# Kernel tuning notes

Hardware: AMD Instinct MI355X
Metric: run time of the kernel (lower is better)

## Reference

```python
import jax, jax.numpy as jnp
import numpy as np

B, L, D, ORDER, POS, HID, LMAX = 4, 4096, 1024, 2, 65, 64, 4096
K2 = (POS - 1) // 2

def _layernorm(x, w, b, eps=1e-5):
    m = jnp.mean(x, -1, keepdims=True)
    v = jnp.mean((x - m) ** 2, -1, keepdims=True)
    return (x - m) * jax.lax.rsqrt(v + eps) * w + b

def _fftconv(x, h, d):
    # torch: rfft(h, 2L, norm='forward') * rfft(x, 2L) -> irfft(.., norm='forward')
    # net scaling equals standard (unnormalized fwd / 1-over-n inverse) circular conv,
    # which is exactly jnp.fft default conventions.
    n = 2 * x.shape[-1]
    y = jnp.fft.irfft(jnp.fft.rfft(x, n=n) * jnp.fft.rfft(h, n=n), n=n)[..., : x.shape[-1]]
    return y + x * d

def setup_inputs() -> dict:
    key = jax.random.key(0)
    ks = jax.random.split(key, 12)
    s = 0.05
    # PositionalEncoding buffers/params (deterministic init, as in torch __init__)
    t = np.linspace(0, 1, LMAX, dtype=np.float64)[:, None]
    t_pos = np.arange(LMAX, dtype=np.float64)[:, None]
    k = np.arange(K2, dtype=np.float64)[None, :]
    z = np.exp(1j * 2 * np.pi * k * t_pos / LMAX)
    pos_z = np.concatenate([t, z.real, z.imag], axis=-1).astype(np.float32)  # (LMAX, POS)
    pos_t = t.reshape(1, 1, LMAX).astype(np.float32)
    # ExponentialDecayWindow alphas (deterministic init)
    max_decay = np.log(0.01) / 0.3
    min_decay = np.log(0.01) / 1.5
    alphas = np.linspace(min_decay, max_decay, D).reshape(1, D, 1).astype(np.float32)
    H3 = (ORDER + 1) * D
    return dict(
        u=jax.random.normal(ks[0], (B, L, D), jnp.float32),
        norm1_w=jnp.ones((D,), jnp.float32), norm1_b=jnp.zeros((D,), jnp.float32),
        proj_w=jax.random.normal(ks[1], (H3, D), jnp.float32) * s,
        proj_b=jnp.zeros((H3,), jnp.float32),
        conv_w=jax.random.normal(ks[2], (H3, 1, 3), jnp.float32) * 0.3,
        conv_b=jnp.zeros((H3,), jnp.float32),
        pos_t=jnp.asarray(pos_t), pos_z=jnp.asarray(pos_z),
        fnn_w0=jax.random.normal(ks[3], (HID, POS), jnp.float32) * s,
        fnn_b0=jnp.zeros((HID,), jnp.float32),
        freq0=8.0 * jnp.ones((1, HID), jnp.float32),
        fnn_w1=jax.random.normal(ks[4], (HID, HID), jnp.float32) * s,
        fnn_b1=jnp.zeros((HID,), jnp.float32),
        freq1=8.0 * jnp.ones((1, HID), jnp.float32),
        fnn_w2=jax.random.normal(ks[5], (HID, HID), jnp.float32) * s,
        fnn_b2=jnp.zeros((HID,), jnp.float32),
        freq2=8.0 * jnp.ones((1, HID), jnp.float32),
        fnn_wout=jax.random.normal(ks[6], (ORDER * D, HID), jnp.float32) * s,
        alphas=jnp.asarray(alphas),
        hy_bias=jax.random.normal(ks[7], (ORDER, 1, D, 1), jnp.float32),
        norm2_w=jnp.ones((D,), jnp.float32), norm2_b=jnp.zeros((D,), jnp.float32),
        fc_w=jax.random.normal(ks[8], (D, D), jnp.float32) * s,
        fc_b=jnp.zeros((D,), jnp.float32),
    )

def reference(u, norm1_w, norm1_b, proj_w, proj_b, conv_w, conv_b, pos_t, pos_z,
              fnn_w0, fnn_b0, freq0, fnn_w1, fnn_b1, freq1, fnn_w2, fnn_b2, freq2,
              fnn_wout, alphas, hy_bias, norm2_w, norm2_b, fc_w, fc_b):
    Lq = u.shape[1]
    # Projection: LN -> Linear -> depthwise short conv (causal-ish, pad=2, slice :L)
    x = _layernorm(u, norm1_w, norm1_b)
    x = jnp.einsum('bld,hd->blh', x, proj_w) + proj_b          # (B,L,3D)
    x = x.transpose(0, 2, 1)                                   # (B,3D,L)
    x = jax.lax.conv_general_dilated(
        x, conv_w, window_strides=(1,), padding=[(2, 2)],
        feature_group_count=x.shape[1],
        dimension_numbers=('NCH', 'OIH', 'NCH'))[..., :Lq] + conv_b[None, :, None]
    # HyenaFilter: sin-MLP over positional features, then exp-decay window
    zf = pos_z[:Lq]                                            # (L,POS)
    h = jnp.sin(freq0 * (zf @ fnn_w0.T + fnn_b0))
    h = jnp.sin(freq1 * (h @ fnn_w1.T + fnn_b1))
    h = jnp.sin(freq2 * (h @ fnn_w2.T + fnn_b2))
    h = (h @ fnn_wout.T).T.reshape(ORDER, D, Lq)               # (order,D,L)
    decay = jnp.exp(alphas * pos_t[..., :Lq])                  # (1,D,L)
    h = h * decay
    # order-wise gated FFT long convolution (faithful to torch chunk/broadcast semantics)
    v = x[:, -1:, :]                                           # (B,1,L)
    for i in range(ORDER):
        v = x[:, i:i + 1, :] * _fftconv(v, h[i][None], hy_bias[i])  # (B,D,L)
    y = u + v.transpose(0, 2, 1)
    out = _layernorm(y, norm2_w, norm2_b) @ fc_w.T + fc_b      # activation = identity
    return out + y
```

## Files before the change

kernel.cpp:

```cpp
#include <hip/hip_runtime.h>
#include <hip/hip_bf16.h>

#define LL 4096
#define DD 1024
#define NB 4
#define N4 4096
#define KBINS 4097
#define NSLOT4 4366
#define PI_F 3.14159265358979323846f
#define INV4 (1.0f / 4096.0f)

typedef __attribute__((ext_vector_type(4))) float f32x4;
typedef __attribute__((ext_vector_type(8))) short s16x8;

#if defined(__has_builtin)
#if __has_builtin(__builtin_amdgcn_global_load_lds)
#define USE_GLOAD_LDS 1
#endif
#endif
#ifndef USE_GLOAD_LDS
#define USE_GLOAD_LDS 0
#endif

__device__ __forceinline__ unsigned short f2bf(float f) {
  unsigned int x = __float_as_uint(f);
  x += 0x7fffu + ((x >> 16) & 1u);
  return (unsigned short)(x >> 16);
}

__device__ __forceinline__ int SLT(int n) { return n + (n >> 4) + (n >> 8); }
__device__ __forceinline__ int brev12(int n) { return (int)(__brev((unsigned)n) >> 20); }

__device__ __forceinline__ float2 cmul(float2 a, float2 b) {
  return make_float2(a.x * b.x - a.y * b.y, a.x * b.y + a.y * b.x);
}
__device__ __forceinline__ float2 cadd(float2 a, float2 b) { return make_float2(a.x + b.x, a.y + b.y); }
__device__ __forceinline__ float2 csub(float2 a, float2 b) { return make_float2(a.x - b.x, a.y - b.y); }
__device__ __forceinline__ float2 conjf(float2 a) { return make_float2(a.x, -a.y); }
__device__ __forceinline__ float2 mulni(float2 v) { return make_float2(v.y, -v.x); }
__device__ __forceinline__ float2 mulpi(float2 v) { return make_float2(-v.y, v.x); }

template<bool INV>
__device__ __forceinline__ void bfly8(float2& A0, float2& A1, float2& A2, float2& A3,
                                      float2& A4, float2& A5, float2& A6, float2& A7,
                                      float2 w1, float2 w2, float2 w3) {
  const float C8 = 0.70710678118654752f;
  float2 t;
  t = cmul(w1, A1); float2 b0 = cadd(A0, t), b1 = csub(A0, t);
  t = cmul(w1, A3); float2 b2 = cadd(A2, t), b3 = csub(A2, t);
  t = cmul(w1, A5); float2 b4 = cadd(A4, t), b5 = csub(A4, t);
  t = cmul(w1, A7); float2 b6 = cadd(A6, t), b7 = csub(A6, t);
  t = cmul(w2, b2);                     float2 c0 = cadd(b0, t), c2 = csub(b0, t);
  t = cmul(w2, b3); t = INV ? mulpi(t) : mulni(t);
  float2 c1 = cadd(b1, t), c3 = csub(b1, t);
  t = cmul(w2, b6);                     float2 c4 = cadd(b4, t), c6 = csub(b4, t);
  t = cmul(w2, b7); t = INV ? mulpi(t) : mulni(t);
  float2 c5 = cadd(b5, t), c7 = csub(b5, t);
  t = cmul(w3, c4); A0 = cadd(c0, t); A4 = csub(c0, t);
  float2 e1 = cmul(w3, c5);
  t = INV ? make_float2(C8 * (e1.x - e1.y), C8 * (e1.y + e1.x))
          : make_float2(C8 * (e1.x + e1.y), C8 * (e1.y - e1.x));
  A1 = cadd(c1, t); A5 = csub(c1, t);
  float2 e2 = cmul(w3, c6); t = INV ? mulpi(e2) : mulni(e2);
  A2 = cadd(c2, t); A6 = csub(c2, t);
  float2 e3 = cmul(w3, c7);
  t = INV ? make_float2(-C8 * (e3.x + e3.y), C8 * (e3.x - e3.y))
          : make_float2(C8 * (e3.y - e3.x), -C8 * (e3.x + e3.y));
  A3 = cadd(c3, t); A7 = csub(c3, t);
}

template<bool INV>
__device__ __forceinline__ void fft4k_01(float2* Z, const float2* __restrict__ tw) {
  const int tid = threadIdx.x;
#pragma unroll
  for (int p = 0; p < 3; ++p) {
    const int hs = 3 * p;
    const int h = 1 << hs;
    const int j0 = tid & (h - 1);
    const int i = ((tid >> hs) << (hs + 3)) + j0;
    int s0 = SLT(i),         s1 = SLT(i + h),     s2 = SLT(i + 2 * h), s3 = SLT(i + 3 * h);
    int s4 = SLT(i + 4 * h), s5 = SLT(i + 5 * h), s6 = SLT(i + 6 * h), s7 = SLT(i + 7 * h);
    float2 a0 = Z[s0], a1 = Z[s1], a2 = Z[s2], a3 = Z[s3];
    float2 a4 = Z[s4], a5 = Z[s5], a6 = Z[s6], a7 = Z[s7];
    float2 w1 = tw[j0 << (12 - hs)];
    float2 w2 = tw[j0 << (11 - hs)];
    float2 w3 = tw[j0 << (10 - hs)];
    if (INV) { w1.y = -w1.y; w2.y = -w2.y; w3.y = -w3.y; }
    bfly8<INV>(a0, a1, a2, a3, a4, a5, a6, a7, w1, w2, w3);
    Z[s0] = a0; Z[s1] = a1; Z[s2] = a2; Z[s3] = a3;
    Z[s4] = a4; Z[s5] = a5; Z[s6] = a6; Z[s7] = a7;
    __builtin_amdgcn_wave_barrier();
  }
}

template<bool INV>
__device__ __forceinline__ void fft4k_p3(const float2* Z, const float2* __restrict__ tw,
                                         float2 d[8]) {
  const int t = threadIdx.x;
#pragma unroll
  for (int k = 0; k < 8; ++k) d[k] = Z[SLT(t + 512 * k)];
  float2 w1 = tw[t << 3], w2 = tw[t << 2], w3 = tw[t << 1];
  if (INV) { w1.y = -w1.y; w2.y = -w2.y; w3.y = -w3.y; }
  bfly8<INV>(d[0], d[1], d[2], d[3], d[4], d[5], d[6], d[7], w1, w2, w3);
}

__global__ void k_prep(float2* tw, const float* __restrict__ fcw,
                       unsigned short* __restrict__ fcwb) {
  const int bid = blockIdx.x;
  if (bid < 16) {
    int k = bid * 256 + threadIdx.x;
    float ang = -2.0f * PI_F * (float)k / 8192.0f;
    float s, c;
    sincosf(ang, &s, &c);
    tw[k] = make_float2(c, s);
  } else {
    int i = (bid - 16) * 256 + threadIdx.x;
    float4 v = ((const float4*)fcw)[i];
    ushort4 o;
    o.x = f2bf(v.x); o.y = f2bf(v.y); o.z = f2bf(v.z); o.w = f2bf(v.w);
    ((ushort4*)fcwb)[i] = o;
  }
}

__global__ __launch_bounds__(256) void k_lnproj_ffn(
    const float* __restrict__ u, const float* __restrict__ n1w, const float* __restrict__ n1b,
    const float* __restrict__ pw, const float* __restrict__ pb,
    float* __restrict__ xp0, float* __restrict__ xp1, float* __restrict__ xpL,
    const float* __restrict__ pos_z,
    const float* __restrict__ w0, const float* __restrict__ b0, const float* __restrict__ f0,
    const float* __restrict__ w1, const float* __restrict__ b1, const float* __restrict__ f1,
    const float* __restrict__ w2, const float* __restrict__ b2, const float* __restrict__ f2,
    float* __restrict__ hid2T) {
  __shared__ float zin[4][66];
  __shared__ float hbuf[4][64];
  const int g = threadIdx.x >> 6, lane = threadIdx.x & 63;
  if (blockIdx.x < (NB * LL) / 4) {
    const int r = blockIdx.x * 4 + g;
    const float* ur = u + (size_t)r * DD;
    float4 uv[4];
    float s = 0.f, sq = 0.f;
#pragma unroll
    for (int c = 0; c < 4; ++c) {
      uv[c] = ((const float4*)ur)[lane + 64 * c];
      s += uv[c].x + uv[c].y + uv[c].z + uv[c].w;
      sq += uv[c].x * uv[c].x + uv[c].y * uv[c].y + uv[c].z * uv[c].z + uv[c].w * uv[c].w;
    }
    for (int m = 1; m < 64; m <<= 1) { s += __shfl_xor(s, m); sq += __shfl_xor(sq, m); }
    const float mean = s * (1.0f / DD);
    const float var = sq * (1.0f / DD) - mean * mean;
    const float rs = rsqrtf(var + 1e-5f);
    float d0 = 0.f, d1 = 0.f, dL = 0.f;
    const float* pwL = pw + (size_t)3071 * DD;
#pragma unroll
    for (int c = 0; c < 4; ++c) {
      int i4 = lane + 64 * c;
      float4 wv = ((const float4*)n1w)[i4];
      float4 bv = ((const float4*)n1b)[i4];
      float4 p0 = ((const float4*)pw)[i4];
      float4 p1v = ((const float4*)(pw + DD))[i4];
      float4 pLv = ((const float4*)pwL)[i4];
      float xn;
      xn = (uv[c].x - mean) * rs * wv.x + bv.x; d0 += xn * p0.x; d1 += xn * p1v.x; dL += xn * pLv.x;
      xn = (uv[c].y - mean) * rs * wv.y + bv.y; d0 += xn * p0.y; d1 += xn * p1v.y; dL += xn * pLv.y;
      xn = (uv[c].z - mean) * rs * wv.z + bv.z; d0 += xn * p0.z; d1 += xn * p1v.z; dL += xn * pLv.z;
      xn = (uv[c].w - mean) * rs * wv.w + bv.w; d0 += xn * p0.w; d1 += xn * p1v.w; dL += xn * pLv.w;
    }
    for (int m = 1; m < 64; m <<= 1) {
      d0 += __shfl_xor(d0, m); d1 += __shfl_xor(d1, m); dL += __shfl_xor(dL, m);
    }
    if (lane == 0) {
      xp0[r] = d0 + pb[0];
      xp1[r] = d1 + pb[1];
      xpL[r] = dL + pb[3071];
    }
  } else {
    const int l0 = (blockIdx.x - (NB * LL) / 4) * 16;
    for (int it = 0; it < 4; ++it) {
      const int l = l0 + g * 4 + it;
      zin[g][lane] = pos_z[(size_t)l * 65 + lane];
      if (lane == 0) zin[g][64] = pos_z[(size_t)l * 65 + 64];
      __syncthreads();
      float acc = b0[lane];
#pragma unroll
      for (int k = 0; k < 65; ++k) acc += zin[g][k] * w0[lane * 65 + k];
      float hv = sinf(f0[lane] * acc);
      __syncthreads();
      hbuf[g][lane] = hv;
      __syncthreads();
      acc = b1[lane];
#pragma unroll
      for (int k = 0; k < 64; ++k) acc += hbuf[g][k] * w1[lane * 64 + k];
      hv = sinf(f1[lane] * acc);
      __syncthreads();
      hbuf[g][lane] = hv;
      __syncthreads();
      acc = b2[lane];
#pragma unroll
      for (int k = 0; k < 64; ++k) acc += hbuf[g][k] * w2[lane * 64 + k];
      hv = sinf(f2[lane] * acc);
      hid2T[(size_t)lane * LL + l] = hv;
      __syncthreads();
    }
  }
}

__global__ __launch_bounds__(256) void k_tapconv(
    const float* __restrict__ xp0, const float* __restrict__ xp1, const float* __restrict__ xpL,
    const float* __restrict__ cw, const float* __restrict__ cb,
    float* __restrict__ x0c, float* __restrict__ x1c, float* __restrict__ xLc) {
  int idx = blockIdx.x * 256 + threadIdx.x;
  if (idx >= NB * LL) return;
  int l = idx & (LL - 1);
  int base = idx - l;
  {
    const float* a = xp0 + base;
    float v = cw[2] * a[l];
    if (l >= 1) v += cw[1] * a[l - 1];
    if (l >= 2) v += cw[0] * a[l - 2];
    x0c[idx] = v + cb[0];
  }
  {
    const float* a = xp1 + base;
    float v = cw[5] * a[l];
    if (l >= 1) v += cw[4] * a[l - 1];
    if (l >= 2) v += cw[3] * a[l - 2];
    x1c[idx] = v + cb[1];
  }
  {
    const float* a = xpL + base;
    float v = cw[3071 * 3 + 2] * a[l];
    if (l >= 1) v += cw[3071 * 3 + 1] * a[l - 1];
    if (l >= 2) v += cw[3071 * 3 + 0] * a[l - 2];
    xLc[idx] = v + cb[3071];
  }
}

__global__ __launch_bounds__(512, 4) void k_fft_filters(
    const float* __restrict__ hid2T, const float* __restrict__ wout,
    const float* __restrict__ alphas, const float* __restrict__ pos_t,
    const float* __restrict__ xLc, float2* __restrict__ Hs, float2* __restrict__ V0s,
    const float2* __restrict__ tw) {
  __shared__ float2 Z[NSLOT4];
  __shared__ float wd[64];
  const int tid = threadIdx.x;
  float2* Out;
  if (blockIdx.x < 2048) {
    const int i = blockIdx.x >> 10, d = blockIdx.x & 1023;
    if (tid < 64) wd[tid] = wout[(size_t)(i * DD + d) * 64 + tid];
    __syncthreads();
    const float ad = alphas[d];
    const float2* h2 = (const float2*)hid2T;
    const float2* pt2 = (const float2*)pos_t;
#pragma unroll
    for (int gi = 0; gi < 4; ++gi) {
      int j = tid + gi * 512;
      float2 acc = make_float2(0.f, 0.f);
#pragma unroll 16
      for (int k = 0; k < 64; ++k) {
        float2 hv = h2[(size_t)k * 2048 + j];
        acc.x = fmaf(hv.x, wd[k], acc.x);
        acc.y = fmaf(hv.y, wd[k], acc.y);
      }
      float2 tt = pt2[j];
      float2 val = make_float2(acc.x * expf(ad * tt.x), acc.y * expf(ad * tt.y));
      int r = brev12(j);
      Z[SLT(r)] = val;
      Z[SLT(r + 1)] = make_float2(0.f, 0.f);
    }
    Out = Hs + ((size_t)i * DD + d) * KBINS;
  } else {
    const int b = blockIdx.x - 2048;
    const float2* src = (const float2*)(xLc + (size_t)b * LL);
#pragma unroll
    for (int gi = 0; gi < 4; ++gi) {
      int j = tid + gi * 512;
      float2 v = src[j];
      int r = brev12(j);
      Z[SLT(r)] = v;
      Z[SLT(r + 1)] = make_float2(0.f, 0.f);
    }
    Out = V0s + (size_t)b * KBINS;
  }
  __syncthreads();
  fft4k_01<false>(Z, tw);
  __syncthreads();
  float2 dd[8];
  fft4k_p3<false>(Z, tw, dd);
#pragma unroll
  for (int k = 0; k < 8; ++k) Z[SLT(tid + 512 * k)] = dd[k];
  __syncthreads();
#pragma unroll
  for (int gi = 0; gi < 4; ++gi) {
    int k = tid + gi * 512;
    float2 zk = Z[SLT(k)];
    float2 zm = Z[SLT((N4 - k) & (N4 - 1))];
    float2 B = conjf(zm);
    float2 E = make_float2(0.5f * (zk.x + B.x), 0.5f * (zk.y + B.y));
    float2 F = make_float2(0.5f * (zk.x - B.x), 0.5f * (zk.y - B.y));
    float2 G = cmul(tw[k], F);
    float2 WO = mulni(G);
    Out[k] = cadd(E, WO);
    Out[N4 - k] = conjf(csub(E, WO));
  }
  if (tid == 0) {
    float2 zc = Z[SLT(2048)];
    float2 F = make_float2(0.f, zc.y);
    float2 G = cmul(tw[2048], F);
    Out[2048] = cadd(make_float2(zc.x, 0.f), mulni(G));
  }
}

__global__ __launch_bounds__(512, 4) void k_conv12(
    const float2* __restrict__ Hs, const float2* __restrict__ V0s,
    const float* __restrict__ x0c, const float* __restrict__ x1c, const float* __restrict__ xLc,
    const float* __restrict__ hyb, float* __restrict__ v2, const float2* __restrict__ tw) {
  __shared__ float2 Z[NSLOT4];
  const int b = blockIdx.x >> 10, d = blockIdx.x & 1023;
  const int tid = threadIdx.x;
  const float2* H0 = Hs + (size_t)d * KBINS;
  const float2* H1 = Hs + (size_t)(DD + d) * KBINS;
  const float2* V = V0s + (size_t)b * KBINS;
  const float2* g0 = (const float2*)(x0c + (size_t)b * LL);
  const float2* g1 = (const float2*)(x1c + (size_t)b * LL);
  const float2* v0 = (const float2*)(xLc + (size_t)b * LL);
  float2 gg0[4], vv0[4];
#pragma unroll
  for (int k = 0; k < 4; ++k) {
    int j = tid + 512 * k;
    gg0[k] = g0[j];
    vv0[k] = v0[j];
  }
#pragma unroll
  for (int gi = 0; gi < 4; ++gi) {
    int k = tid + gi * 512;
    int m = N4 - k;
    float2 Yk = cmul(V[k], H0[k]);
    float2 Ym = cmul(V[m], H0[m]);
    float2 B = conjf(Ym);
    float2 E = make_float2(0.5f * (Yk.x + B.x), 0.5f * (Yk.y + B.y));
    float2 F = make_float2(0.5f * (Yk.x - B.x), 0.5f * (Yk.y - B.y));
    float2 O = cmul(conjf(tw[k]), F);
    float2 iO = mulpi(O);
    Z[SLT(brev12(k))] = cadd(E, iO);
    if (k > 0) Z[SLT(brev12(m))] = conjf(csub(E, iO));
  }
  if (tid == 0) {
    float2 A = cmul(V[2048], H0[2048]);
    float2 F = make_float2(0.f, A.y);
    float2 O = cmul(conjf(tw[2048]), F);
    Z[SLT(brev12(2048))] = cadd(make_float2(A.x, 0.f), mulpi(O));
  }
  __syncthreads();
  fft4k_01<true>(Z, tw);
  __syncthreads();
  float2 dA[8];
  fft4k_p3<true>(Z, tw, dA);
  const float bd0 = hyb[d], bd1 = hyb[DD + d];
  float2 vsave[4];
#pragma unroll
  for (int k = 0; k < 4; ++k) {
    vsave[k] = make_float2(gg0[k].x * fmaf(dA[k].x, INV4, bd0 * vv0[k].x),
                           gg0[k].y * fmaf(dA[k].y, INV4, bd0 * vv0[k].y));
  }
  __syncthreads();
#pragma unroll
  for (int k = 0; k < 4; ++k) {
    int j = tid + 512 * k;
    int r = brev12(j);
    Z[SLT(r)] = vsave[k];
    Z[SLT(r + 1)] = make_float2(0.f, 0.f);
  }
  __syncthreads();
  fft4k_01<false>(Z, tw);
  __syncthreads();
  float2 dB[8];
  fft4k_p3<false>(Z, tw, dB);
#pragma unroll
  for (int k = 0; k < 8; ++k) Z[SLT(tid + 512 * k)] = dB[k];
  __syncthreads();
  float2 gg1[4];
#pragma unroll
  for (int k = 0; k < 4; ++k) gg1[k] = g1[tid + 512 * k];
  float2 zpk[4], zpm[4], z2048;
#pragma unroll
  for (int gi = 0; gi < 4; ++gi) {
    int k = tid + gi * 512;
    int m = N4 - k;
    float2 zk = Z[SLT(k)];
    float2 zm = Z[SLT(m & (N4 - 1))];
    float2 B = conjf(zm);
    float2 E = make_float2(0.5f * (zk.x + B.x), 0.5f * (zk.y + B.y));
    float2 F = make_float2(0.5f * (zk.x - B.x), 0.5f * (zk.y - B.y));
    float2 wk = tw[k];
    float2 G = cmul(wk, F);
    float2 WO = mulni(G);
    float2 Xk = cadd(E, WO);
    float2 Xm = conjf(csub(E, WO));
    float2 Yk = cmul(Xk, H1[k]);
    float2 Ym = cmul(Xm, H1[m]);
    float2 B2 = conjf(Ym);
    float2 E2 = make_float2(0.5f * (Yk.x + B2.x), 0.5f * (Yk.y + B2.y));
    float2 F2 = make_float2(0.5f * (Yk.x - B2.x), 0.5f * (Yk.y - B2.y));
    float2 O2 = cmul(conjf(wk), F2);
    float2 iO2 = mulpi(O2);
    zpk[gi] = cadd(E2, iO2);
    zpm[gi] = conjf(csub(E2, iO2));
  }
  if (tid == 0) {
    float2 zc = Z[SLT(2048)];
    float2 F = make_float2(0.f, zc.y);
    float2 G = cmul(tw[2048], F);
    float2 Xk = cadd(make_float2(zc.x, 0.f), mulni(G));
    float2 Y = cmul(Xk, H1[2048]);
    float2 F2 = make_float2(0.f, Y.y);
    float2 O2 = cmul(conjf(tw[2048]), F2);
    z2048 = cadd(make_float2(Y.x, 0.f), mulpi(O2));
  }
  __syncthreads();
#pragma unroll
  for (int gi = 0; gi < 4; ++gi) {
    int k = tid + gi * 512;
    Z[SLT(brev12(k))] = zpk[gi];
    if (k > 0) Z[SLT(brev12(N4 - k))] = zpm[gi];
  }
  if (tid == 0) Z[SLT(brev12(2048))] = z2048;
  __syncthreads();
  fft4k_01<true>(Z, tw);
  __syncthreads();
  float2 dC[8];
  fft4k_p3<true>(Z, tw, dC);
  float2* out2 = (float2*)(v2 + ((size_t)b * DD + d) * LL);
#pragma unroll
  for (int k = 0; k < 4; ++k) {
    int j = tid + 512 * k;
    out2[j] = make_float2(gg1[k].x * fmaf(dC[k].x, INV4, bd1 * vsave[k].x),
                          gg1[k].y * fmaf(dC[k].y, INV4, bd1 * vsave[k].y));
  }
}

__global__ __launch_bounds__(256) void k_transpose_add(const float* __restrict__ v2,
                                                       const float* __restrict__ u,
                                                       float* __restrict__ y) {
  __shared__ float T[64][65];
  const int bid = blockIdx.x;
  const int lt = bid & 63, dt = (bid >> 6) & 15, b = bid >> 10;
  const int t = threadIdx.x;
  const int tdr = t >> 2, lc0 = (t & 3) * 16;
  const float* vp = v2 + ((size_t)(b * DD + dt * 64 + tdr)) * LL + lt * 64 + lc0;
#pragma unroll
  for (int q = 0; q < 4; ++q) {
    float4 vv = ((const float4*)vp)[q];
    T[tdr][lc0 + 4 * q + 0] = vv.x;
    T[tdr][lc0 + 4 * q + 1] = vv.y;
    T[tdr][lc0 + 4 * q + 2] = vv.z;
    T[tdr][lc0 + 4 * q + 3] = vv.w;
  }
  __syncthreads();
  const int dc = t & 63, lg = t >> 6;
#pragma unroll
  for (int lr0 = 0; lr0 < 64; lr0 += 4) {
    int lr = lr0 + lg;
    size_t idx = ((size_t)b * LL + lt * 64 + lr) * DD + dt * 64 + dc;
    y[idx] = u[idx] + T[dc][lr];
  }
}

__global__ __launch_bounds__(256) void k_ln2(const float* __restrict__ y,
                                             const float* __restrict__ w,
                                             const float* __restrict__ bb,
                                             unsigned short* __restrict__ yln) {
  const int wid = threadIdx.x >> 6, lane = threadIdx.x & 63;
  const size_t r = (size_t)blockIdx.x * 4 + wid;
  const float* yr = y + r * DD;
  float4 v[4];
  float s = 0.f, sq = 0.f;
#pragma unroll
  for (int c = 0; c < 4; ++c) {
    v[c] = ((const float4*)yr)[lane + 64 * c];
    s += v[c].x + v[c].y + v[c].z + v[c].w;
    sq += v[c].x * v[c].x + v[c].y * v[c].y + v[c].z * v[c].z + v[c].w * v[c].w;
  }
  for (int m = 1; m < 64; m <<= 1) { s += __shfl_xor(s, m); sq += __shfl_xor(sq, m); }
  const float mean = s * (1.0f / DD);
  const float var = sq * (1.0f / DD) - mean * mean;
  const float rs = rsqrtf(var + 1e-5f);
#pragma unroll
  for (int c = 0; c < 4; ++c) {
    int i4 = lane + 64 * c;
    float4 wv = ((const float4*)w)[i4];
    float4 bv = ((const float4*)bb)[i4];
    ushort4 o;
    o.x = f2bf((v[c].x - mean) * rs * wv.x + bv.x);
    o.y = f2bf((v[c].y - mean) * rs * wv.y + bv.y);
    o.z = f2bf((v[c].z - mean) * rs * wv.z + bv.z);
    o.w = f2bf((v[c].w - mean) * rs * wv.w + bv.w);
    ((ushort4*)(yln + r * DD))[i4] = o;
  }
}

#define GBM 128
#define GBN 128
#define GBK 64
#if USE_GLOAD_LDS
#define LDK 64
#else
#define LDK 72
#endif

__global__ __launch_bounds__(256) void k_gemm(const short* __restrict__ A,
                                              const short* __restrict__ Bw,
                                              const float* __restrict__ fcb,
                                              const float* __restrict__ yy,
                                              float* __restrict__ out) {
  __shared__ short As[GBM * LDK];
  __shared__ short Bs[GBN * LDK];
  const int t = threadIdx.x;
  const int bm = blockIdx.x & 127;
  const int bn = blockIdx.x >> 7;
  const int wave = t >> 6, lane = t & 63;
  const int wr = wave >> 1, wc = wave & 1;
  const int rrow = lane & 15, kb = (lane >> 4) * 8;

  f32x4 acc[4][4];
#pragma unroll
  for (int i = 0; i < 4; ++i)
#pragma unroll
    for (int j = 0; j < 4; ++j) acc[i][j] = (f32x4){0.f, 0.f, 0.f, 0.f};

  const size_t abase = (size_t)(bm * GBM) * 1024;
  const size_t bbase = (size_t)(bn * GBN) * 1024;

  for (int k0 = 0; k0 < 1024; k0 += GBK) {
#if USE_GLOAD_LDS
    {
      const int r0 = wave * 32;
      const int lrow = lane >> 3, loff = (lane & 7) * 8;
#pragma unroll
      for (int q = 0; q < 4; ++q) {
        const int row = r0 + 8 * q + lrow;
        __builtin_amdgcn_global_load_lds(
            (const __attribute__((address_space(1))) void*)(A + abase + (size_t)row * 1024 + k0 + loff),
            (__attribute__((address_space(3))) void*)&As[(r0 + 8 * q) * LDK], 16, 0, 0);
        __builtin_amdgcn_global_load_lds(
            (const __attribute__((address_space(1))) void*)(Bw + bbase + (size_t)row * 1024 + k0 + loff),
            (__attribute__((address_space(3))) void*)&Bs[(r0 + 8 * q) * LDK], 16, 0, 0);
      }
    }
#else
#pragma unroll
    for (int c = 0; c < 4; ++c) {
      int chunk = c * 256 + t;
      int row = chunk >> 3, off = (chunk & 7) * 8;
      s16x8 av = *(const s16x8*)(A + abase + (size_t)row * 1024 + k0 + off);
      *(s16x8*)&As[row * LDK + off] = av;
      s16x8 bv = *(const s16x8*)(Bw + bbase + (size_t)row * 1024 + k0 + off);
      *(s16x8*)&Bs[row * LDK + off] = bv;
    }
#endif
    __syncthreads();
    s16x8 af[2][4], bfr[2][4];
#pragma unroll
    for (int ks = 0; ks < 2; ++ks) {
#pragma unroll
      for (int mr = 0; mr < 4; ++mr)
        af[ks][mr] = *(const s16x8*)&As[(wr * 64 + mr * 16 + rrow) * LDK + ks * 32 + kb];
#pragma unroll
      for (int nc = 0; nc < 4; ++nc)
        bfr[ks][nc] = *(const s16x8*)&Bs[(wc * 64 + nc * 16 + rrow) * LDK + ks * 32 + kb];
    }
#pragma unroll
    for (int ks = 0; ks < 2; ++ks)
#pragma unroll
      for (int mr = 0; mr < 4; ++mr)
#pragma unroll
        for (int nc = 0; nc < 4; ++nc)
          acc[mr][nc] = __builtin_amdgcn_mfma_f32_16x16x32_bf16(af[ks][mr], bfr[ks][nc],
                                                                acc[mr][nc], 0, 0, 0);
    __syncthreads();
  }
  const int cg = lane >> 4, cr = lane & 15;
#pragma unroll
  for (int mr = 0; mr < 4; ++mr)
#pragma unroll
    for (int nc = 0; nc < 4; ++nc) {
      f32x4 a = acc[mr][nc];
      int col = bn * GBN + wc * 64 + nc * 16 + cr;
#pragma unroll
      for (int q = 0; q < 4; ++q) {
        int row = bm * GBM + wr * 64 + mr * 16 + cg * 4 + q;
        size_t idx = (size_t)row * 1024 + col;
        out[idx] = a[q] + fcb[col] + yy[idx];
      }
    }
}

extern "C" void kernel_launch(void* const* d_in, const int* in_sizes, int n_in,
                              void* d_out, int out_size, void* d_ws, size_t ws_size,
                              hipStream_t stream) {
  const float* u      = (const float*)d_in[0];
  const float* n1w    = (const float*)d_in[1];
  const float* n1b    = (const float*)d_in[2];
  const float* projw  = (const float*)d_in[3];
  const float* projb  = (const float*)d_in[4];
  const float* convw  = (const float*)d_in[5];
  const float* convb  = (const float*)d_in[6];
  const float* pos_t  = (const float*)d_in[7];
  const float* pos_z  = (const float*)d_in[8];
  const float* w0     = (const float*)d_in[9];
  const float* b0     = (const float*)d_in[10];
  const float* f0     = (const float*)d_in[11];
  const float* w1     = (const float*)d_in[12];
  const float* b1     = (const float*)d_in[13];
  const float* f1     = (const float*)d_in[14];
  const float* w2     = (const float*)d_in[15];
  const float* b2     = (const float*)d_in[16];
  const float* f2     = (const float*)d_in[17];
  const float* wout   = (const float*)d_in[18];
  const float* alphas = (const float*)d_in[19];
  const float* hyb    = (const float*)d_in[20];
  const float* n2w    = (const float*)d_in[21];
  const float* n2b    = (const float*)d_in[22];
  const float* fcw    = (const float*)d_in[23];
  const float* fcb    = (const float*)d_in[24];

  char* wsb = (char*)d_ws;
  size_t off = 0;
  auto alloc = [&](size_t bytes) -> void* {
    off = (off + 255) & ~(size_t)255;
    void* p = wsb + off;
    off += bytes;
    return p;
  };
  float2* tw    = (float2*)alloc(sizeof(float2) * 4096);
  float*  xp0   = (float*)alloc(sizeof(float) * NB * LL);
  float*  xp1   = (float*)alloc(sizeof(float) * NB * LL);
  float*  xpL   = (float*)alloc(sizeof(float) * NB * LL);
  float*  x0c   = (float*)alloc(sizeof(float) * NB * LL);
  float*  x1c   = (float*)alloc(sizeof(float) * NB * LL);
  float*  xLc   = (float*)alloc(sizeof(float) * NB * LL);
  float*  hid2T = (float*)alloc(sizeof(float) * 64 * LL);
  float2* Hs    = (float2*)alloc(sizeof(float2) * 2 * DD * KBINS);
  float2* V0s   = (float2*)alloc(sizeof(float2) * NB * KBINS);
  float*  v2    = (float*)alloc(sizeof(float) * NB * DD * LL);
  unsigned short* fcwb = (unsigned short*)alloc(sizeof(unsigned short) * DD * DD);
  float*          y   = (float*)Hs;
  unsigned short* yln = (unsigned short*)v2;
  (void)ws_size; (void)in_sizes; (void)n_in; (void)out_size;

  k_prep<<<16 + (DD * DD / 4) / 256, 256, 0, stream>>>(tw, fcw, fcwb);
  k_lnproj_ffn<<<(NB * LL) / 4 + LL / 16, 256, 0, stream>>>(
      u, n1w, n1b, projw, projb, xp0, xp1, xpL,
      pos_z, w0, b0, f0, w1, b1, f1, w2, b2, f2, hid2T);
  k_tapconv<<<(NB * LL) / 256, 256, 0, stream>>>(xp0, xp1, xpL, convw, convb, x0c, x1c, xLc);
  k_fft_filters<<<2048 + NB, 512, 0, stream>>>(hid2T, wout, alphas, pos_t, xLc, Hs, V0s, tw);
  k_conv12<<<NB * DD, 512, 0, stream>>>(Hs, V0s, x0c, x1c, xLc, hyb, v2, tw);
  k_transpose_add<<<4096, 256, 0, stream>>>(v2, u, y);
  k_ln2<<<(NB * LL) / 4, 256, 0, stream>>>(y, n2w, n2b, yln);
  k_gemm<<<(16384 / GBM) * (1024 / GBN), 256, 0, stream>>>((const short*)yln, (const short*)fcwb,
                                                           fcb, y, (float*)d_out);
}
```

Measured before the change: 445.1 us.

## Split filter MLP output projection into a register-tiled GEMM kernel before FFT

Moves the filter output projection (hid2T times wout) and exp-decay window out of the FFT kernel into a separate kernel. Each thread computes 16 channels by 4 positions, so every hid2T element loaded is reused across 16 channels instead of being reloaded once per channel block. The result (2048x4096 floats) is written to the v2 scratch buffer and read back by the simplified FFT kernel. In exchange it adds an extra launch and about 32 MB of global write plus read traffic.

```diff
diff --git a/kernel.cpp b/kernel.cpp
--- a/kernel.cpp
+++ b/kernel.cpp
@@ -235,51 +235,65 @@
   }
 }
 
-__global__ __launch_bounds__(512, 4) void k_fft_filters(
+#define FG_CH 16
+__global__ __launch_bounds__(256) void k_filter_gemm(
     const float* __restrict__ hid2T, const float* __restrict__ wout,
     const float* __restrict__ alphas, const float* __restrict__ pos_t,
-    const float* __restrict__ xLc, float2* __restrict__ Hs, float2* __restrict__ V0s,
-    const float2* __restrict__ tw) {
+    float* __restrict__ h) {
+  __shared__ float wdl[FG_CH][64];
+  const int cg = blockIdx.x & 127;
+  const int lg = blockIdx.x >> 7;
+  const int t = threadIdx.x;
+  for (int idx = t; idx < FG_CH * 64; idx += 256) {
+    int c = idx >> 6, k = idx & 63;
+    wdl[c][k] = wout[(size_t)(cg * FG_CH + c) * 64 + k];
+  }
+  __syncthreads();
+  const int l0 = lg * 1024 + 4 * t;
+  float4 acc[FG_CH];
+#pragma unroll
+  for (int c = 0; c < FG_CH; ++c) acc[c] = make_float4(0.f, 0.f, 0.f, 0.f);
+  for (int k = 0; k < 64; ++k) {
+    float4 hv = *(const float4*)&hid2T[(size_t)k * LL + l0];
+#pragma unroll
+    for (int c = 0; c < FG_CH; ++c) {
+      acc[c].x = fmaf(hv.x, wdl[c][k], acc[c].x);
+      acc[c].y = fmaf(hv.y, wdl[c][k], acc[c].y);
+      acc[c].z = fmaf(hv.z, wdl[c][k], acc[c].z);
+      acc[c].w = fmaf(hv.w, wdl[c][k], acc[c].w);
+    }
+  }
+  float4 tt = *(const float4*)&pos_t[l0];
+#pragma unroll
+  for (int c = 0; c < FG_CH; ++c) {
+    int ch = cg * FG_CH + c;
+    float a = alphas[ch & (DD - 1)];
+    float4 o;
+    o.x = acc[c].x * expf(a * tt.x);
+    o.y = acc[c].y * expf(a * tt.y);
+    o.z = acc[c].z * expf(a * tt.z);
+    o.w = acc[c].w * expf(a * tt.w);
+    *(float4*)&h[(size_t)ch * LL + l0] = o;
+  }
+}
+
+__global__ __launch_bounds__(512, 4) void k_fft_filters(
+    const float* __restrict__ h, const float* __restrict__ xLc,
+    float2* __restrict__ Hs, float2* __restrict__ V0s, const float2* __restrict__ tw) {
   __shared__ float2 Z[NSLOT4];
-  __shared__ float wd[64];
   const int tid = threadIdx.x;
-  float2* Out;
-  if (blockIdx.x < 2048) {
-    const int i = blockIdx.x >> 10, d = blockIdx.x & 1023;
-    if (tid < 64) wd[tid] = wout[(size_t)(i * DD + d) * 64 + tid];
-    __syncthreads();
-    const float ad = alphas[d];
-    const float2* h2 = (const float2*)hid2T;
-    const float2* pt2 = (const float2*)pos_t;
-#pragma unroll
-    for (int gi = 0; gi < 4; ++gi) {
-      int j = tid + gi * 512;
-      float2 acc = make_float2(0.f, 0.f);
-#pragma unroll 16
-      for (int k = 0; k < 64; ++k) {
-        float2 hv = h2[(size_t)k * 2048 + j];
-        acc.x = fmaf(hv.x, wd[k], acc.x);
-        acc.y = fmaf(hv.y, wd[k], acc.y);
-      }
-      float2 tt = pt2[j];
-      float2 val = make_float2(acc.x * expf(ad * tt.x), acc.y * expf(ad * tt.y));
-      int r = brev12(j);
-      Z[SLT(r)] = val;
-      Z[SLT(r + 1)] = make_float2(0.f, 0.f);
-    }
-    Out = Hs + ((size_t)i * DD + d) * KBINS;
-  } else {
-    const int b = blockIdx.x - 2048;
-    const float2* src = (const float2*)(xLc + (size_t)b * LL);
-#pragma unroll
-    for (int gi = 0; gi < 4; ++gi) {
-      int j = tid + gi * 512;
-      float2 v = src[j];
-      int r = brev12(j);
-      Z[SLT(r)] = v;
-      Z[SLT(r + 1)] = make_float2(0.f, 0.f);
-    }
-    Out = V0s + (size_t)b * KBINS;
+  const int bid = blockIdx.x;
+  const float2* src = (bid < 2048) ? (const float2*)(h + (size_t)bid * LL)
+                                   : (const float2*)(xLc + (size_t)(bid - 2048) * LL);
+  float2* Out = (bid < 2048) ? (Hs + (size_t)bid * KBINS)
+                             : (V0s + (size_t)(bid - 2048) * KBINS);
+#pragma unroll
+  for (int gi = 0; gi < 4; ++gi) {
+    int j = tid + gi * 512;
+    float2 v = src[j];
+    int r = brev12(j);
+    Z[SLT(r)] = v;
+    Z[SLT(r + 1)] = make_float2(0.f, 0.f);
   }
   __syncthreads();
   fft4k_01<false>(Z, tw);
@@ -645,6 +659,7 @@
   unsigned short* fcwb = (unsigned short*)alloc(sizeof(unsigned short) * DD * DD);
   float*          y   = (float*)Hs;
   unsigned short* yln = (unsigned short*)v2;
+  float*          h   = v2;
   (void)ws_size; (void)in_sizes; (void)n_in; (void)out_size;
 
   k_prep<<<16 + (DD * DD / 4) / 256, 256, 0, stream>>>(tw, fcw, fcwb);
@@ -652,7 +667,8 @@
       u, n1w, n1b, projw, projb, xp0, xp1, xpL,
       pos_z, w0, b0, f0, w1, b1, f1, w2, b2, f2, hid2T);
   k_tapconv<<<(NB * LL) / 256, 256, 0, stream>>>(xp0, xp1, xpL, convw, convb, x0c, x1c, xLc);
-  k_fft_filters<<<2048 + NB, 512, 0, stream>>>(hid2T, wout, alphas, pos_t, xLc, Hs, V0s, tw);
+  k_filter_gemm<<<512, 256, 0, stream>>>(hid2T, wout, alphas, pos_t, h);
+  k_fft_filters<<<2048 + NB, 512, 0, stream>>>(h, xLc, Hs, V0s, tw);
   k_conv12<<<NB * DD, 512, 0, stream>>>(Hs, V0s, x0c, x1c, xLc, hyb, v2, tw);
   k_transpose_add<<<4096, 256, 0, stream>>>(v2, u, y);
   k_ln2<<<(NB * LL) / 4, 256, 0, stream>>>(y, n2w, n2b, yln);
```

Result: faster. 367.7 us (-17.4%).
